# Optimization experiments

Measured on AMD Instinct MI355X. Metric: run time of the kernel, lower is better.

## Reference

```python
import jax, jax.numpy as jnp
import numpy as np

TEMP = 1.0  # composition softmax temperature

def _bank_topk(x, U, V, logits, top_k):
    # softmax over primitive logits, select top-k, renormalize, fused low-rank projection
    w = jax.nn.softmax(logits / TEMP)                     # [P]
    tw, ti = jax.lax.top_k(w, top_k)                      # [k], [k]
    tw = tw / tw.sum()
    Us = U[ti]                                            # [k, d_in, r]
    Vs = V[ti]                                            # [k, r, d_out]
    h = jnp.einsum('bsd,kdr->bksr', x, Us)                # low-rank bottleneck
    return jnp.einsum('bksr,kro,k->bso', h, Vs, tw)       # weighted fuse

def reference(x, q_U, q_V, k_U, k_V, v_U, v_V, q_logits, k_logits, v_logits, out_w, top_k):
    B, S, _ = x.shape
    H, D = 16, 64
    q = _bank_topk(x, q_U, q_V, q_logits, top_k)
    k = _bank_topk(x, k_U, k_V, k_logits, top_k)
    v = _bank_topk(x, v_U, v_V, v_logits, top_k)
    q = q.reshape(B, S, H, D).transpose(0, 2, 1, 3)       # [B,H,S,D]
    k = k.reshape(B, S, H, D).transpose(0, 2, 1, 3)
    v = v.reshape(B, S, H, D).transpose(0, 2, 1, 3)
    scale = 1.0 / jnp.sqrt(jnp.asarray(D, dtype=x.dtype))
    scores = jnp.einsum('bhqd,bhkd->bhqk', q, k) * scale  # [B,H,S,S]
    causal = jnp.triu(jnp.ones((S, S), dtype=bool), 1)
    scores = jnp.where(causal[None, None], jnp.finfo(x.dtype).min, scores)
    probs = jax.nn.softmax(scores, axis=-1)
    out = jnp.einsum('bhqk,bhkd->bhqd', probs, v)
    out = out.transpose(0, 2, 1, 3).reshape(B, S, H * D)
    return out @ out_w.T                                   # nn.Linear(H*D, d_model, bias=False)

def setup_inputs() -> dict:
    key = jax.random.key(0)
    ks = jax.random.split(key, 11)
    P, d, r = 16, 1024, 64
    B, S = 4, 1024
    f = jnp.float32
    inp = {
        'x': jax.random.normal(ks[0], (B, S, d), f),
        'q_U': jax.random.normal(ks[1], (P, d, r), f) * (1.0 / np.sqrt(d)),
        'q_V': jax.random.normal(ks[2], (P, r, d), f) * (1.0 / np.sqrt(r)),
        'k_U': jax.random.normal(ks[3], (P, d, r), f) * (1.0 / np.sqrt(d)),
        'k_V': jax.random.normal(ks[4], (P, r, d), f) * (1.0 / np.sqrt(r)),
        'v_U': jax.random.normal(ks[5], (P, d, r), f) * (1.0 / np.sqrt(d)),
        'v_V': jax.random.normal(ks[6], (P, r, d), f) * (1.0 / np.sqrt(r)),
        'q_logits': jax.random.normal(ks[7], (P,), f) * 0.01,
        'k_logits': jax.random.normal(ks[8], (P,), f) * 0.01,
        'v_logits': jax.random.normal(ks[9], (P,), f) * 0.01,
        'out_w': jax.random.normal(ks[10], (d, d), f) * (1.0 / np.sqrt(d)),
        'top_k': 4,
    }
    return inp
```

## Files before the change

kernel.cpp:

```cpp
#include <hip/hip_runtime.h>
#include <math.h>

#define D_MODEL 1024
#define RANK    64
#define PMAX    16
#define S_LEN   1024
#define HD      64
#define MROWS   4096
#define NHEAD   16
#define BATCH   4

typedef short short8v __attribute__((ext_vector_type(8)));
typedef float floatx4 __attribute__((ext_vector_type(4)));

typedef __attribute__((address_space(1))) const unsigned int* gptr_t;
typedef __attribute__((address_space(3))) unsigned int* lptr_t;

static __device__ __forceinline__ void async16(const void* g, void* l) {
    __builtin_amdgcn_global_load_lds((gptr_t)g, (lptr_t)l, 16, 0, 0);
}

static __device__ __forceinline__ short f2bf(float f) {
    unsigned int u = __float_as_uint(f);
    u = (u + 0x7fffu + ((u >> 16) & 1u)) >> 16;
    return (short)u;
}

__global__ void topk_weights_kernel(const float* __restrict__ ql,
                                    const float* __restrict__ kl,
                                    const float* __restrict__ vl,
                                    const int* __restrict__ topk,
                                    int* __restrict__ idx_out,
                                    float* __restrict__ w_out) {
    int bank = threadIdx.x;
    if (bank >= 3) return;
    const float* lg = (bank == 0) ? ql : (bank == 1) ? kl : vl;
    int K = *topk; if (K < 1) K = 1; if (K > PMAX) K = PMAX;
    float l[PMAX];
    for (int i = 0; i < PMAX; ++i) l[i] = lg[i];
    bool used[PMAX];
    for (int i = 0; i < PMAX; ++i) used[i] = false;
    int   sel_i[PMAX];
    float sel_l[PMAX];
    for (int j = 0; j < K; ++j) {
        int best = -1; float bv = -INFINITY;
        for (int i = 0; i < PMAX; ++i)
            if (!used[i] && l[i] > bv) { bv = l[i]; best = i; }
        used[best] = true; sel_i[j] = best; sel_l[j] = bv;
    }
    float mx = sel_l[0];
    float e[PMAX];
    float sum = 0.f;
    for (int j = 0; j < K; ++j) { e[j] = __expf(sel_l[j] - mx); sum += e[j]; }
    float inv = 1.f / sum;
    for (int j = 0; j < PMAX; ++j) {
        idx_out[bank * PMAX + j] = (j < K) ? sel_i[j] : 0;
        w_out[bank * PMAX + j]   = (j < K) ? e[j] * inv : 0.f;
    }
}

__global__ __launch_bounds__(256) void convert_bf16_kernel(
    const float* __restrict__ src, short* __restrict__ dst, int n4) {
    int i = blockIdx.x * 256 + threadIdx.x;
    if (i < n4) {
        float4 f = ((const float4*)src)[i];
        short4 o;
        o.x = f2bf(f.x); o.y = f2bf(f.y); o.z = f2bf(f.z); o.w = f2bf(f.w);
        ((short4*)dst)[i] = o;
    }
}

__global__ __launch_bounds__(256) void prep_uv_kernel(
    const float* __restrict__ qU, const float* __restrict__ kU,
    const float* __restrict__ vU,
    const float* __restrict__ qV, const float* __restrict__ kV,
    const float* __restrict__ vV,
    const int* __restrict__ idx, const float* __restrict__ wsel,
    short* __restrict__ Ut, short* __restrict__ Vt) {
    int z    = blockIdx.z;
    int j    = blockIdx.y;
    int tile = blockIdx.x;
    int t    = threadIdx.x;
    __shared__ float T[64][65];
    int bank = (z < 3) ? z : z - 3;
    int p = idx[bank * PMAX + j];

    if (z < 3) {
        const float* U = (bank == 0) ? qU : (bank == 1) ? kU : vU;
        const float* src = U + (size_t)p * D_MODEL * RANK;
        int d0 = tile * 64;
        int rl = t & 63, dq = t >> 6;
#pragma unroll
        for (int i = 0; i < 16; ++i) {
            int dl = i * 4 + dq;
            T[rl][dl] = src[(size_t)(d0 + dl) * RANK + rl];
        }
        __syncthreads();
        short* dst = Ut + (size_t)bank * D_MODEL * D_MODEL;
        int rr = t >> 2;
#pragma unroll
        for (int i = 0; i < 4; ++i) {
            int c = (t & 3) * 16 + i * 4;
            short4 o;
            o.x = f2bf(T[rr][c + 0]); o.y = f2bf(T[rr][c + 1]);
            o.z = f2bf(T[rr][c + 2]); o.w = f2bf(T[rr][c + 3]);
            *(short4*)&dst[(size_t)(j * 64 + rr) * D_MODEL + d0 + c] = o;
        }
    } else {
        const float* V = (bank == 0) ? qV : (bank == 1) ? kV : vV;
        float wj = wsel[bank * PMAX + j];
        const float* src = V + (size_t)p * RANK * D_MODEL;
        int n0 = tile * 64;
        int nl = t & 63, rq = t >> 6;
#pragma unroll
        for (int i = 0; i < 16; ++i) {
            int rl = i * 4 + rq;
            T[nl][rl] = src[(size_t)rl * D_MODEL + n0 + nl] * wj;
        }
        __syncthreads();
        short* dst = Vt + (size_t)bank * D_MODEL * D_MODEL;
        int rr = t >> 2;
#pragma unroll
        for (int i = 0; i < 4; ++i) {
            int c = (t & 3) * 16 + i * 4;
            short4 o;
            o.x = f2bf(T[rr][c + 0]); o.y = f2bf(T[rr][c + 1]);
            o.z = f2bf(T[rr][c + 2]); o.w = f2bf(T[rr][c + 3]);
            *(short4*)&dst[(size_t)(n0 + rr) * D_MODEL + j * 64 + c] = o;
        }
    }
}

static __device__ __forceinline__ void mfma_gemm_tile(
    const short* __restrict__ A, const short* __restrict__ B, int kl,
    int m0, int n0, short* As, short* Bs, floatx4 acc[4][4]) {
    const int t    = threadIdx.x;
    const int w    = t >> 6;
    const int lane = t & 63;
    const int wm   = w & 1, wn = w >> 1;
    const int colL = lane & 15, quad = lane >> 4;
    const int srow  = lane >> 2;
    const int skoff = (lane & 3) * 8;

#pragma unroll
    for (int i = 0; i < 4; ++i)
#pragma unroll
        for (int j = 0; j < 4; ++j) acc[i][j] = (floatx4){0.f, 0.f, 0.f, 0.f};

    for (int k0 = 0; k0 < kl; k0 += 32) {
        async16(A + (size_t)(m0 + w * 16 + srow) * D_MODEL + k0 + skoff,
                As + (w * 16 + srow) * 32 + skoff);
        async16(A + (size_t)(m0 + 64 + w * 16 + srow) * D_MODEL + k0 + skoff,
                As + (64 + w * 16 + srow) * 32 + skoff);
        async16(B + (size_t)(n0 + w * 16 + srow) * D_MODEL + k0 + skoff,
                Bs + (w * 16 + srow) * 32 + skoff);
        async16(B + (size_t)(n0 + 64 + w * 16 + srow) * D_MODEL + k0 + skoff,
                Bs + (64 + w * 16 + srow) * 32 + skoff);
        __syncthreads();
        short8v af[4], bf[4];
#pragma unroll
        for (int i = 0; i < 4; ++i)
            af[i] = *(const short8v*)&As[(wm * 64 + i * 16 + colL) * 32 + quad * 8];
#pragma unroll
        for (int j = 0; j < 4; ++j)
            bf[j] = *(const short8v*)&Bs[(wn * 64 + j * 16 + colL) * 32 + quad * 8];
#pragma unroll
        for (int i = 0; i < 4; ++i)
#pragma unroll
            for (int j = 0; j < 4; ++j)
                acc[i][j] = __builtin_amdgcn_mfma_f32_16x16x32_bf16(af[i], bf[j], acc[i][j], 0, 0, 0);
        __syncthreads();
    }
}

__global__ __launch_bounds__(256) void gemm_h_kernel(
    const short* __restrict__ xb, const short* __restrict__ Ut,
    const int* __restrict__ topk, short* __restrict__ h) {
    int K = *topk; if (K < 1) K = 1; if (K > PMAX) K = PMAX;
    int n0 = blockIdx.y * 128;
    if (n0 >= K * 64) return;
    int m0 = blockIdx.x * 128;
    int bank = blockIdx.z;
    __shared__ short As[128 * 32];
    __shared__ short Bs[128 * 32];
    floatx4 acc[4][4];
    mfma_gemm_tile(xb, Ut + (size_t)bank * D_MODEL * D_MODEL, D_MODEL, m0, n0, As, Bs, acc);

    const int t = threadIdx.x, w = t >> 6, lane = t & 63;
    const int wm = w & 1, wn = w >> 1, colL = lane & 15, quad = lane >> 4;
    short* H = h + (size_t)bank * MROWS * D_MODEL;
#pragma unroll
    for (int i = 0; i < 4; ++i)
#pragma unroll
        for (int j = 0; j < 4; ++j)
#pragma unroll
            for (int r = 0; r < 4; ++r)
                H[(size_t)(m0 + wm * 64 + i * 16 + quad * 4 + r) * D_MODEL +
                  (n0 + wn * 64 + j * 16 + colL)] = f2bf(acc[i][j][r]);
}

__global__ __launch_bounds__(256) void gemm_qkv_kernel(
    const short* __restrict__ h, const short* __restrict__ Vt,
    const int* __restrict__ topk, short* __restrict__ qkv) {
    int K = *topk; if (K < 1) K = 1; if (K > PMAX) K = PMAX;
    int m0 = blockIdx.x * 128;
    int n0 = blockIdx.y * 128;
    int bank = blockIdx.z;
    __shared__ short As[128 * 32];
    __shared__ short Bs[128 * 32];
    floatx4 acc[4][4];
    mfma_gemm_tile(h + (size_t)bank * MROWS * D_MODEL,
                   Vt + (size_t)bank * D_MODEL * D_MODEL, K * 64, m0, n0, As, Bs, acc);

    const int t = threadIdx.x, w = t >> 6, lane = t & 63;
    const int wm = w & 1, wn = w >> 1, colL = lane & 15, quad = lane >> 4;
    short* outp = qkv + (size_t)bank * MROWS * D_MODEL;
    const float scl = (bank == 0) ? 0.18033688f : 1.0f;
#pragma unroll
    for (int i = 0; i < 4; ++i)
#pragma unroll
        for (int j = 0; j < 4; ++j)
#pragma unroll
            for (int r = 0; r < 4; ++r) {
                int m = m0 + wm * 64 + i * 16 + quad * 4 + r;
                int n = n0 + wn * 64 + j * 16 + colL;
                int b = m >> 10, s = m & 1023;
                int head = n >> 6, d = n & 63;
                outp[(((size_t)(b * NHEAD + head) << 10) + s) * HD + d] = f2bf(acc[i][j][r] * scl);
            }
}

__global__ __launch_bounds__(256) void transpose_v_kernel(
    const short* __restrict__ src, short* __restrict__ dst) {
    int st = blockIdx.x, bh = blockIdx.y;
    __shared__ short T[64][72];
    const short* S = src + (size_t)bh * (S_LEN * HD) + (size_t)st * 64 * HD;
    int r = threadIdx.x >> 2, i = threadIdx.x & 3;
    *(short8v*)&T[r][i * 16]     = *(const short8v*)&S[r * HD + i * 16];
    *(short8v*)&T[r][i * 16 + 8] = *(const short8v*)&S[r * HD + i * 16 + 8];
    __syncthreads();
    short* Drow = dst + (size_t)bh * (S_LEN * HD) + (size_t)r * S_LEN + st * 64 + i * 16;
    short8v o0, o1;
#pragma unroll
    for (int k = 0; k < 8; ++k) o0[k] = T[i * 16 + k][r];
#pragma unroll
    for (int k = 0; k < 8; ++k) o1[k] = T[i * 16 + 8 + k][r];
    *(short8v*)&Drow[0] = o0;
    *(short8v*)&Drow[8] = o1;
}

static __device__ __forceinline__ void stage_tiles(
    const short* __restrict__ Kg, const short* __restrict__ Vg, int jt,
    short* KsB, short* VsB, int w, int lane) {
#pragma unroll
    for (int q = 0; q < 2; ++q) {
        int c   = q * 64 + lane;
        int r16 = c >> 3;
        int i   = c & 7;
        int r   = w * 16 + r16;
        int g   = i ^ (r16 & 7);
        async16(Kg + (size_t)(jt * 64 + r) * HD + g * 8, KsB + r * 64 + i * 8);
        async16(Vg + (size_t)r * S_LEN + jt * 64 + g * 8, VsB + r * 64 + i * 8);
    }
}

template<bool DIAG>
static __device__ __forceinline__ void attn_step(
    const short* KsB, const short* VsB, short* Pw,
    short8v aq0, short8v aq1, int w, int col, int quad,
    floatx4& O0, floatx4& O1, floatx4& O2, floatx4& O3,
    float mrow[4], float lrow[4]) {
    const int colLow = col & 7;
    floatx4 c4[4];
#pragma unroll
    for (int n = 0; n < 4; ++n) {
        if (!DIAG || n <= w) {
            floatx4 z = {0.f, 0.f, 0.f, 0.f};
            short8v b0 = *(const short8v*)&KsB[(n * 16 + col) * 64 + ((quad ^ colLow) << 3)];
            short8v b1 = *(const short8v*)&KsB[(n * 16 + col) * 64 + (((quad + 4) ^ colLow) << 3)];
            z = __builtin_amdgcn_mfma_f32_16x16x32_bf16(aq0, b0, z, 0, 0, 0);
            z = __builtin_amdgcn_mfma_f32_16x16x32_bf16(aq1, b1, z, 0, 0, 0);
            if (DIAG) {
#pragma unroll
                for (int r = 0; r < 4; ++r)
                    if (n == w && col > quad * 4 + r) z[r] = -INFINITY;
            }
            c4[n] = z;
        } else {
            c4[n] = (floatx4){-INFINITY, -INFINITY, -INFINITY, -INFINITY};
        }
    }
#pragma unroll
    for (int r = 0; r < 4; ++r) {
        float tm = fmaxf(fmaxf(c4[0][r], c4[1][r]), fmaxf(c4[2][r], c4[3][r]));
        tm = fmaxf(tm, __shfl_xor(tm, 1));
        tm = fmaxf(tm, __shfl_xor(tm, 2));
        tm = fmaxf(tm, __shfl_xor(tm, 4));
        tm = fmaxf(tm, __shfl_xor(tm, 8));
        float mnew  = fmaxf(mrow[r], tm);
        float alpha = exp2f(mrow[r] - mnew);
        float p0 = exp2f(c4[0][r] - mnew), p1 = exp2f(c4[1][r] - mnew);
        float p2 = exp2f(c4[2][r] - mnew), p3 = exp2f(c4[3][r] - mnew);
        lrow[r] = lrow[r] * alpha + (p0 + p1 + p2 + p3);
        mrow[r] = mnew;
        O0[r] *= alpha; O1[r] *= alpha; O2[r] *= alpha; O3[r] *= alpha;
        short* pr = Pw + (quad * 4 + r) * 72 + col;
        pr[0]  = f2bf(p0); pr[16] = f2bf(p1);
        pr[32] = f2bf(p2); pr[48] = f2bf(p3);
    }
    const int ksmax = DIAG ? (w >> 1) : 1;
#pragma unroll
    for (int ks = 0; ks < 2; ++ks) {
        if (ks > ksmax) break;
        short8v ap = *(const short8v*)&Pw[col * 72 + ks * 32 + quad * 8];
        int pc = ((ks * 4 + quad) ^ colLow) << 3;
        short8v v0 = *(const short8v*)&VsB[(0  + col) * 64 + pc];
        short8v v1 = *(const short8v*)&VsB[(16 + col) * 64 + pc];
        short8v v2 = *(const short8v*)&VsB[(32 + col) * 64 + pc];
        short8v v3 = *(const short8v*)&VsB[(48 + col) * 64 + pc];
        O0 = __builtin_amdgcn_mfma_f32_16x16x32_bf16(ap, v0, O0, 0, 0, 0);
        O1 = __builtin_amdgcn_mfma_f32_16x16x32_bf16(ap, v1, O1, 0, 0, 0);
        O2 = __builtin_amdgcn_mfma_f32_16x16x32_bf16(ap, v2, O2, 0, 0, 0);
        O3 = __builtin_amdgcn_mfma_f32_16x16x32_bf16(ap, v3, O3, 0, 0, 0);
    }
}

__global__ __launch_bounds__(256) void attn_mfma_kernel(
    const short* __restrict__ qkv,
    const short* __restrict__ vtb,
    short* __restrict__ attn_out) {
    const int t    = threadIdx.x;
    const int w    = t >> 6;
    const int lane = t & 63;
    const int col  = lane & 15;
    const int quad = lane >> 4;
    const int pr   = blockIdx.x;
    const int bh   = blockIdx.y;
    const size_t HS   = (size_t)S_LEN * HD;
    const size_t BSTR = (size_t)MROWS * D_MODEL;
    const short* Qg = qkv + (size_t)bh * HS;
    const short* Kg = qkv + BSTR + (size_t)bh * HS;
    const short* Vg = vtb + (size_t)bh * HS;

    __shared__ short Ks[2][4096];
    __shared__ short Vs[2][4096];
    __shared__ short Ps[4][16 * 72];
    short* Pw = &Ps[w][0];

    for (int ph = 0; ph < 2; ++ph) {
        const int qt = ph ? (15 - pr) : pr;
        const int qrow = qt * 64 + w * 16 + col;
        short8v aq0 = *(const short8v*)(Qg + (size_t)qrow * HD + quad * 8);
        short8v aq1 = *(const short8v*)(Qg + (size_t)qrow * HD + 32 + quad * 8);
        floatx4 O0 = {0.f, 0.f, 0.f, 0.f}, O1 = O0, O2 = O0, O3 = O0;
        float mrow[4] = {-INFINITY, -INFINITY, -INFINITY, -INFINITY};
        float lrow[4] = {0.f, 0.f, 0.f, 0.f};

        __syncthreads();
        stage_tiles(Kg, Vg, 0, Ks[0], Vs[0], w, lane);
        __syncthreads();
        int cur = 0;
        for (int jt = 0; jt < qt; ++jt) {
            stage_tiles(Kg, Vg, jt + 1, Ks[cur ^ 1], Vs[cur ^ 1], w, lane);
            attn_step<false>(Ks[cur], Vs[cur], Pw, aq0, aq1, w, col, quad,
                             O0, O1, O2, O3, mrow, lrow);
            __syncthreads();
            cur ^= 1;
        }
        attn_step<true>(Ks[cur], Vs[cur], Pw, aq0, aq1, w, col, quad,
                        O0, O1, O2, O3, mrow, lrow);

        const int b  = bh >> 4;
        const int hh = bh & 15;
        short* orow = attn_out +
            ((size_t)(b * S_LEN) + qt * 64 + w * 16) * D_MODEL + hh * 64;
#pragma unroll
        for (int r = 0; r < 4; ++r) {
            float l = lrow[r];
            l += __shfl_xor(l, 1); l += __shfl_xor(l, 2);
            l += __shfl_xor(l, 4); l += __shfl_xor(l, 8);
            float inv = 1.f / l;
            short* prw = orow + (size_t)(quad * 4 + r) * D_MODEL;
            prw[0  + col] = f2bf(O0[r] * inv);
            prw[16 + col] = f2bf(O1[r] * inv);
            prw[32 + col] = f2bf(O2[r] * inv);
            prw[48 + col] = f2bf(O3[r] * inv);
        }
    }
}

__global__ __launch_bounds__(256) void gemm_proj_kernel(
    const short* __restrict__ attnb, const short* __restrict__ wb,
    float* __restrict__ outp) {
    int m0 = blockIdx.x * 128;
    int n0 = blockIdx.y * 128;
    __shared__ short As[128 * 32];
    __shared__ short Bs[128 * 32];
    floatx4 acc[4][4];
    mfma_gemm_tile(attnb, wb, D_MODEL, m0, n0, As, Bs, acc);

    const int t = threadIdx.x, w = t >> 6, lane = t & 63;
    const int wm = w & 1, wn = w >> 1, colL = lane & 15, quad = lane >> 4;
#pragma unroll
    for (int i = 0; i < 4; ++i)
#pragma unroll
        for (int j = 0; j < 4; ++j)
#pragma unroll
            for (int r = 0; r < 4; ++r)
                outp[(size_t)(m0 + wm * 64 + i * 16 + quad * 4 + r) * D_MODEL +
                     (n0 + wn * 64 + j * 16 + colL)] = acc[i][j][r];
}

extern "C" void kernel_launch(void* const* d_in, const int* in_sizes, int n_in,
                              void* d_out, int out_size, void* d_ws, size_t ws_size,
                              hipStream_t stream) {
    const float* x    = (const float*)d_in[0];
    const float* qU   = (const float*)d_in[1];
    const float* qV   = (const float*)d_in[2];
    const float* kU   = (const float*)d_in[3];
    const float* kV   = (const float*)d_in[4];
    const float* vU   = (const float*)d_in[5];
    const float* vV   = (const float*)d_in[6];
    const float* qlg  = (const float*)d_in[7];
    const float* klg  = (const float*)d_in[8];
    const float* vlg  = (const float*)d_in[9];
    const float* outw = (const float*)d_in[10];
    const int*   topk = (const int*)d_in[11];
    float* outp = (float*)d_out;

    char* ws = (char*)d_ws;
    int*   idxp = (int*)ws;
    float* wp   = (float*)(ws + 256);
    short* xb   = (short*)(ws + 512);
    short* Ut   = xb + (size_t)MROWS * D_MODEL;
    short* Vt   = Ut + (size_t)3 * D_MODEL * D_MODEL;
    short* wb   = Vt + (size_t)3 * D_MODEL * D_MODEL;
    short* hbuf = wb + (size_t)D_MODEL * D_MODEL;
    short* qkvb = hbuf + (size_t)3 * MROWS * D_MODEL;
    short* attnb = qkvb + (size_t)3 * MROWS * D_MODEL;
    short* vtb  = attnb + (size_t)MROWS * D_MODEL;

    topk_weights_kernel<<<1, 64, 0, stream>>>(qlg, klg, vlg, topk, idxp, wp);
    convert_bf16_kernel<<<(MROWS * D_MODEL / 4 + 255) / 256, 256, 0, stream>>>(
        x, xb, MROWS * D_MODEL / 4);
    convert_bf16_kernel<<<(D_MODEL * D_MODEL / 4 + 255) / 256, 256, 0, stream>>>(
        outw, wb, D_MODEL * D_MODEL / 4);
    prep_uv_kernel<<<dim3(16, 16, 6), 256, 0, stream>>>(
        qU, kU, vU, qV, kV, vV, idxp, wp, Ut, Vt);
    gemm_h_kernel<<<dim3(32, 8, 3), 256, 0, stream>>>(xb, Ut, topk, hbuf);
    gemm_qkv_kernel<<<dim3(32, 8, 3), 256, 0, stream>>>(hbuf, Vt, topk, qkvb);
    transpose_v_kernel<<<dim3(16, 64), 256, 0, stream>>>(
        qkvb + (size_t)2 * MROWS * D_MODEL, vtb);
    attn_mfma_kernel<<<dim3(8, 64), 256, 0, stream>>>(qkvb, vtb, attnb);
    gemm_proj_kernel<<<dim3(32, 8), 256, 0, stream>>>(attnb, wb, outp);
}
```

Baseline: 231.3 us.

## Fuse prep kernels, double-buffer GEMM tiles, and widen attention key chunks

Merges the top-k selection, both bf16 conversions and the U/V preparation into one launch, with each prep block recomputing its own top-k choice so the separate topk kernel goes away. The GEMM main loop is double-buffered, prefetching the next K slice into a second LDS buffer while MFMAs run on the current one. The attention kernel now processes 128-key chunks per stage instead of 64, with a new V layout and swizzle. Together these cut launch count and per-step barriers, at the cost of twice the LDS per block, which may lower occupancy.

New measurement: 252.6 us. 9.2% more time.

```diff
diff --git a/kernel.cpp b/kernel.cpp
--- a/kernel.cpp
+++ b/kernel.cpp
@@ -26,65 +26,70 @@
     return (short)u;
 }
 
-__global__ void topk_weights_kernel(const float* __restrict__ ql,
-                                    const float* __restrict__ kl,
-                                    const float* __restrict__ vl,
-                                    const int* __restrict__ topk,
-                                    int* __restrict__ idx_out,
-                                    float* __restrict__ w_out) {
-    int bank = threadIdx.x;
-    if (bank >= 3) return;
-    const float* lg = (bank == 0) ? ql : (bank == 1) ? kl : vl;
-    int K = *topk; if (K < 1) K = 1; if (K > PMAX) K = PMAX;
+static __device__ __forceinline__ void topk_select(
+    const float* __restrict__ lg, int K, int j, int* p_out, float* w_out) {
     float l[PMAX];
+#pragma unroll
     for (int i = 0; i < PMAX; ++i) l[i] = lg[i];
     bool used[PMAX];
+#pragma unroll
     for (int i = 0; i < PMAX; ++i) used[i] = false;
-    int   sel_i[PMAX];
-    float sel_l[PMAX];
-    for (int j = 0; j < K; ++j) {
+    float first = 0.f, sum = 0.f, sl = 0.f;
+    int sel = 0;
+    for (int jj = 0; jj < K; ++jj) {
         int best = -1; float bv = -INFINITY;
         for (int i = 0; i < PMAX; ++i)
             if (!used[i] && l[i] > bv) { bv = l[i]; best = i; }
-        used[best] = true; sel_i[j] = best; sel_l[j] = bv;
-    }
-    float mx = sel_l[0];
-    float e[PMAX];
-    float sum = 0.f;
-    for (int j = 0; j < K; ++j) { e[j] = __expf(sel_l[j] - mx); sum += e[j]; }
-    float inv = 1.f / sum;
-    for (int j = 0; j < PMAX; ++j) {
-        idx_out[bank * PMAX + j] = (j < K) ? sel_i[j] : 0;
-        w_out[bank * PMAX + j]   = (j < K) ? e[j] * inv : 0.f;
-    }
-}
-
-__global__ __launch_bounds__(256) void convert_bf16_kernel(
-    const float* __restrict__ src, short* __restrict__ dst, int n4) {
-    int i = blockIdx.x * 256 + threadIdx.x;
-    if (i < n4) {
-        float4 f = ((const float4*)src)[i];
-        short4 o;
-        o.x = f2bf(f.x); o.y = f2bf(f.y); o.z = f2bf(f.z); o.w = f2bf(f.w);
-        ((short4*)dst)[i] = o;
-    }
-}
-
-__global__ __launch_bounds__(256) void prep_uv_kernel(
+        used[best] = true;
+        if (jj == 0) first = bv;
+        float e = __expf(bv - first);
+        sum += e;
+        if (jj == j) { sel = best; sl = e; }
+    }
+    if (j < K) { *p_out = sel; *w_out = sl / sum; }
+    else       { *p_out = 0;   *w_out = 0.f; }
+}
+
+__global__ __launch_bounds__(256) void prep_all_kernel(
+    const float* __restrict__ x,
     const float* __restrict__ qU, const float* __restrict__ kU,
     const float* __restrict__ vU,
     const float* __restrict__ qV, const float* __restrict__ kV,
     const float* __restrict__ vV,
-    const int* __restrict__ idx, const float* __restrict__ wsel,
+    const float* __restrict__ qlg, const float* __restrict__ klg,
+    const float* __restrict__ vlg,
+    const int* __restrict__ topk, const float* __restrict__ outw,
+    short* __restrict__ xb, short* __restrict__ wb,
     short* __restrict__ Ut, short* __restrict__ Vt) {
-    int z    = blockIdx.z;
-    int j    = blockIdx.y;
-    int tile = blockIdx.x;
-    int t    = threadIdx.x;
+    int b = blockIdx.x;
+    int t = threadIdx.x;
+    if (b < 4096) {
+        int i = b * 256 + t;
+        float4 f = ((const float4*)x)[i];
+        short4 o;
+        o.x = f2bf(f.x); o.y = f2bf(f.y); o.z = f2bf(f.z); o.w = f2bf(f.w);
+        ((short4*)xb)[i] = o;
+        return;
+    }
+    if (b < 5120) {
+        int i = (b - 4096) * 256 + t;
+        float4 f = ((const float4*)outw)[i];
+        short4 o;
+        o.x = f2bf(f.x); o.y = f2bf(f.y); o.z = f2bf(f.z); o.w = f2bf(f.w);
+        ((short4*)wb)[i] = o;
+        return;
+    }
+    int rem  = b - 5120;
+    int z    = rem >> 8;
+    int j    = (rem >> 4) & 15;
+    int tile = rem & 15;
+    int bank = (z < 3) ? z : z - 3;
+    int K = *topk; if (K < 1) K = 1; if (K > PMAX) K = PMAX;
+    const float* lg = (bank == 0) ? qlg : (bank == 1) ? klg : vlg;
+    int p; float wj;
+    topk_select(lg, K, j, &p, &wj);
+
     __shared__ float T[64][65];
-    int bank = (z < 3) ? z : z - 3;
-    int p = idx[bank * PMAX + j];
-
     if (z < 3) {
         const float* U = (bank == 0) ? qU : (bank == 1) ? kU : vU;
         const float* src = U + (size_t)p * D_MODEL * RANK;
@@ -108,7 +113,6 @@
         }
     } else {
         const float* V = (bank == 0) ? qV : (bank == 1) ? kV : vV;
-        float wj = wsel[bank * PMAX + j];
         const float* src = V + (size_t)p * RANK * D_MODEL;
         int n0 = tile * 64;
         int nl = t & 63, rq = t >> 6;
@@ -129,6 +133,20 @@
             *(short4*)&dst[(size_t)(n0 + rr) * D_MODEL + j * 64 + c] = o;
         }
     }
+}
+
+static __device__ __forceinline__ void gemm_stage(
+    const short* __restrict__ A, const short* __restrict__ B,
+    int m0, int n0, int k0, short* Ab, short* Bb,
+    int w, int srow, int skoff) {
+    async16(A + (size_t)(m0 + w * 16 + srow) * D_MODEL + k0 + skoff,
+            Ab + (w * 16 + srow) * 32 + skoff);
+    async16(A + (size_t)(m0 + 64 + w * 16 + srow) * D_MODEL + k0 + skoff,
+            Ab + (64 + w * 16 + srow) * 32 + skoff);
+    async16(B + (size_t)(n0 + w * 16 + srow) * D_MODEL + k0 + skoff,
+            Bb + (w * 16 + srow) * 32 + skoff);
+    async16(B + (size_t)(n0 + 64 + w * 16 + srow) * D_MODEL + k0 + skoff,
+            Bb + (64 + w * 16 + srow) * 32 + skoff);
 }
 
 static __device__ __forceinline__ void mfma_gemm_tile(
@@ -147,29 +165,31 @@
 #pragma unroll
         for (int j = 0; j < 4; ++j) acc[i][j] = (floatx4){0.f, 0.f, 0.f, 0.f};
 
-    for (int k0 = 0; k0 < kl; k0 += 32) {
-        async16(A + (size_t)(m0 + w * 16 + srow) * D_MODEL + k0 + skoff,
-                As + (w * 16 + srow) * 32 + skoff);
-        async16(A + (size_t)(m0 + 64 + w * 16 + srow) * D_MODEL + k0 + skoff,
-                As + (64 + w * 16 + srow) * 32 + skoff);
-        async16(B + (size_t)(n0 + w * 16 + srow) * D_MODEL + k0 + skoff,
-                Bs + (w * 16 + srow) * 32 + skoff);
-        async16(B + (size_t)(n0 + 64 + w * 16 + srow) * D_MODEL + k0 + skoff,
-                Bs + (64 + w * 16 + srow) * 32 + skoff);
-        __syncthreads();
+    gemm_stage(A, B, m0, n0, 0, As, Bs, w, srow, skoff);
+    __syncthreads();
+    const int nk = kl >> 5;
+    int cur = 0;
+    for (int kt = 0; kt < nk; ++kt) {
+        if (kt + 1 < nk)
+            gemm_stage(A, B, m0, n0, (kt + 1) * 32,
+                       As + ((cur ^ 1) << 12), Bs + ((cur ^ 1) << 12),
+                       w, srow, skoff);
+        const short* Ab = As + (cur << 12);
+        const short* Bb = Bs + (cur << 12);
         short8v af[4], bf[4];
 #pragma unroll
         for (int i = 0; i < 4; ++i)
-            af[i] = *(const short8v*)&As[(wm * 64 + i * 16 + colL) * 32 + quad * 8];
+            af[i] = *(const short8v*)&Ab[(wm * 64 + i * 16 + colL) * 32 + quad * 8];
 #pragma unroll
         for (int j = 0; j < 4; ++j)
-            bf[j] = *(const short8v*)&Bs[(wn * 64 + j * 16 + colL) * 32 + quad * 8];
+            bf[j] = *(const short8v*)&Bb[(wn * 64 + j * 16 + colL) * 32 + quad * 8];
 #pragma unroll
         for (int i = 0; i < 4; ++i)
 #pragma unroll
             for (int j = 0; j < 4; ++j)
                 acc[i][j] = __builtin_amdgcn_mfma_f32_16x16x32_bf16(af[i], bf[j], acc[i][j], 0, 0, 0);
         __syncthreads();
+        cur ^= 1;
     }
 }
 
@@ -181,8 +201,8 @@
     if (n0 >= K * 64) return;
     int m0 = blockIdx.x * 128;
     int bank = blockIdx.z;
-    __shared__ short As[128 * 32];
-    __shared__ short Bs[128 * 32];
+    __shared__ short As[8192];
+    __shared__ short Bs[8192];
     floatx4 acc[4][4];
     mfma_gemm_tile(xb, Ut + (size_t)bank * D_MODEL * D_MODEL, D_MODEL, m0, n0, As, Bs, acc);
 
@@ -206,8 +226,8 @@
     int m0 = blockIdx.x * 128;
     int n0 = blockIdx.y * 128;
     int bank = blockIdx.z;
-    __shared__ short As[128 * 32];
-    __shared__ short Bs[128 * 32];
+    __shared__ short As[8192];
+    __shared__ short Bs[8192];
     floatx4 acc[4][4];
     mfma_gemm_tile(h + (size_t)bank * MROWS * D_MODEL,
                    Vt + (size_t)bank * D_MODEL * D_MODEL, K * 64, m0, n0, As, Bs, acc);
@@ -249,79 +269,105 @@
     *(short8v*)&Drow[8] = o1;
 }
 
-static __device__ __forceinline__ void stage_tiles(
-    const short* __restrict__ Kg, const short* __restrict__ Vg, int jt,
+static __device__ __forceinline__ void attn_stage(
+    const short* __restrict__ Kg, const short* __restrict__ Vg, int base,
     short* KsB, short* VsB, int w, int lane) {
 #pragma unroll
-    for (int q = 0; q < 2; ++q) {
-        int c   = q * 64 + lane;
-        int r16 = c >> 3;
-        int i   = c & 7;
-        int r   = w * 16 + r16;
-        int g   = i ^ (r16 & 7);
-        async16(Kg + (size_t)(jt * 64 + r) * HD + g * 8, KsB + r * 64 + i * 8);
-        async16(Vg + (size_t)r * S_LEN + jt * 64 + g * 8, VsB + r * 64 + i * 8);
-    }
-}
-
-template<bool DIAG>
+    for (int q2 = 0; q2 < 4; ++q2) {
+        int row = w * 32 + q2 * 8 + (lane >> 3);
+        int i   = lane & 7;
+        int g   = i ^ (row & 7);
+        async16(Kg + (size_t)(base + row) * HD + g * 8, KsB + row * 64 + i * 8);
+    }
+#pragma unroll
+    for (int q2 = 0; q2 < 4; ++q2) {
+        int d    = w * 16 + q2 * 4 + (lane >> 4);
+        int i    = lane & 15;
+        int half = i >> 3, i3 = i & 7;
+        int g3   = i3 ^ (d & 7);
+        async16(Vg + (size_t)d * S_LEN + base + half * 64 + g3 * 8,
+                VsB + d * 128 + i * 8);
+    }
+}
+
+template<int NN, bool DIAG>
 static __device__ __forceinline__ void attn_step(
     const short* KsB, const short* VsB, short* Pw,
     short8v aq0, short8v aq1, int w, int col, int quad,
     floatx4& O0, floatx4& O1, floatx4& O2, floatx4& O3,
     float mrow[4], float lrow[4]) {
-    const int colLow = col & 7;
-    floatx4 c4[4];
-#pragma unroll
-    for (int n = 0; n < 4; ++n) {
-        if (!DIAG || n <= w) {
+    const int cl7 = col & 7;
+    float sc[NN][4];
+#pragma unroll
+    for (int n = 0; n < NN; ++n) {
+        const int dn = n - (NN - 4);
+        if (DIAG && dn > w) {
+#pragma unroll
+            for (int r = 0; r < 4; ++r) sc[n][r] = -INFINITY;
+        } else {
             floatx4 z = {0.f, 0.f, 0.f, 0.f};
-            short8v b0 = *(const short8v*)&KsB[(n * 16 + col) * 64 + ((quad ^ colLow) << 3)];
-            short8v b1 = *(const short8v*)&KsB[(n * 16 + col) * 64 + (((quad + 4) ^ colLow) << 3)];
+            const short* kb = KsB + (n * 16 + col) * 64;
+            short8v b0 = *(const short8v*)(kb + ((quad ^ cl7) << 3));
+            short8v b1 = *(const short8v*)(kb + (((quad + 4) ^ cl7) << 3));
             z = __builtin_amdgcn_mfma_f32_16x16x32_bf16(aq0, b0, z, 0, 0, 0);
             z = __builtin_amdgcn_mfma_f32_16x16x32_bf16(aq1, b1, z, 0, 0, 0);
-            if (DIAG) {
+            if (DIAG && dn == w) {
 #pragma unroll
                 for (int r = 0; r < 4; ++r)
-                    if (n == w && col > quad * 4 + r) z[r] = -INFINITY;
+                    if (col > quad * 4 + r) z[r] = -INFINITY;
             }
-            c4[n] = z;
-        } else {
-            c4[n] = (floatx4){-INFINITY, -INFINITY, -INFINITY, -INFINITY};
-        }
-    }
+#pragma unroll
+            for (int r = 0; r < 4; ++r) sc[n][r] = z[r];
+        }
+    }
+    float pv[NN][4];
 #pragma unroll
     for (int r = 0; r < 4; ++r) {
-        float tm = fmaxf(fmaxf(c4[0][r], c4[1][r]), fmaxf(c4[2][r], c4[3][r]));
+        float tm = sc[0][r];
+#pragma unroll
+        for (int n = 1; n < NN; ++n) tm = fmaxf(tm, sc[n][r]);
         tm = fmaxf(tm, __shfl_xor(tm, 1));
         tm = fmaxf(tm, __shfl_xor(tm, 2));
         tm = fmaxf(tm, __shfl_xor(tm, 4));
         tm = fmaxf(tm, __shfl_xor(tm, 8));
         float mnew  = fmaxf(mrow[r], tm);
         float alpha = exp2f(mrow[r] - mnew);
-        float p0 = exp2f(c4[0][r] - mnew), p1 = exp2f(c4[1][r] - mnew);
-        float p2 = exp2f(c4[2][r] - mnew), p3 = exp2f(c4[3][r] - mnew);
-        lrow[r] = lrow[r] * alpha + (p0 + p1 + p2 + p3);
+        float ps = 0.f;
+#pragma unroll
+        for (int n = 0; n < NN; ++n) {
+            float p = exp2f(sc[n][r] - mnew);
+            pv[n][r] = p;
+            ps += p;
+        }
+        lrow[r] = lrow[r] * alpha + ps;
         mrow[r] = mnew;
         O0[r] *= alpha; O1[r] *= alpha; O2[r] *= alpha; O3[r] *= alpha;
-        short* pr = Pw + (quad * 4 + r) * 72 + col;
-        pr[0]  = f2bf(p0); pr[16] = f2bf(p1);
-        pr[32] = f2bf(p2); pr[48] = f2bf(p3);
-    }
-    const int ksmax = DIAG ? (w >> 1) : 1;
-#pragma unroll
-    for (int ks = 0; ks < 2; ++ks) {
-        if (ks > ksmax) break;
-        short8v ap = *(const short8v*)&Pw[col * 72 + ks * 32 + quad * 8];
-        int pc = ((ks * 4 + quad) ^ colLow) << 3;
-        short8v v0 = *(const short8v*)&VsB[(0  + col) * 64 + pc];
-        short8v v1 = *(const short8v*)&VsB[(16 + col) * 64 + pc];
-        short8v v2 = *(const short8v*)&VsB[(32 + col) * 64 + pc];
-        short8v v3 = *(const short8v*)&VsB[(48 + col) * 64 + pc];
-        O0 = __builtin_amdgcn_mfma_f32_16x16x32_bf16(ap, v0, O0, 0, 0, 0);
-        O1 = __builtin_amdgcn_mfma_f32_16x16x32_bf16(ap, v1, O1, 0, 0, 0);
-        O2 = __builtin_amdgcn_mfma_f32_16x16x32_bf16(ap, v2, O2, 0, 0, 0);
-        O3 = __builtin_amdgcn_mfma_f32_16x16x32_bf16(ap, v3, O3, 0, 0, 0);
+    }
+#pragma unroll
+    for (int h = 0; h < NN / 4; ++h) {
+#pragma unroll
+        for (int n2 = 0; n2 < 4; ++n2)
+#pragma unroll
+            for (int r = 0; r < 4; ++r)
+                Pw[(quad * 4 + r) * 72 + n2 * 16 + col] = f2bf(pv[h * 4 + n2][r]);
+        const int kslim = DIAG ? ((NN - 4 + w) >> 1) : 3;
+#pragma unroll
+        for (int ks2 = 2 * h; ks2 < 2 * h + 2; ++ks2) {
+            if (DIAG && ks2 > kslim) break;
+            short8v ap = *(const short8v*)(Pw + col * 72 + (ks2 & 1) * 32 + quad * 8);
+            const int half = ks2 >> 1;
+            const int i3   = (ks2 & 1) * 4 + quad;
+            const int swz  = ((i3 ^ cl7) << 3);
+            const short* vb = VsB + half * 64 + swz;
+            short8v v0 = *(const short8v*)(vb + (0  + col) * 128);
+            short8v v1 = *(const short8v*)(vb + (16 + col) * 128);
+            short8v v2 = *(const short8v*)(vb + (32 + col) * 128);
+            short8v v3 = *(const short8v*)(vb + (48 + col) * 128);
+            O0 = __builtin_amdgcn_mfma_f32_16x16x32_bf16(ap, v0, O0, 0, 0, 0);
+            O1 = __builtin_amdgcn_mfma_f32_16x16x32_bf16(ap, v1, O1, 0, 0, 0);
+            O2 = __builtin_amdgcn_mfma_f32_16x16x32_bf16(ap, v2, O2, 0, 0, 0);
+            O3 = __builtin_amdgcn_mfma_f32_16x16x32_bf16(ap, v3, O3, 0, 0, 0);
+        }
     }
 }
 
@@ -342,10 +388,10 @@
     const short* Kg = qkv + BSTR + (size_t)bh * HS;
     const short* Vg = vtb + (size_t)bh * HS;
 
-    __shared__ short Ks[2][4096];
-    __shared__ short Vs[2][4096];
-    __shared__ short Ps[4][16 * 72];
-    short* Pw = &Ps[w][0];
+    __shared__ short Ks[2][8192];
+    __shared__ short Vs[2][8192];
+    __shared__ short Ps[4][1152];
+    short* Pw = Ps[w];
 
     for (int ph = 0; ph < 2; ++ph) {
         const int qt = ph ? (15 - pr) : pr;
@@ -356,19 +402,24 @@
         float mrow[4] = {-INFINITY, -INFINITY, -INFINITY, -INFINITY};
         float lrow[4] = {0.f, 0.f, 0.f, 0.f};
 
+        const int nC = (qt + 2) >> 1;
         __syncthreads();
-        stage_tiles(Kg, Vg, 0, Ks[0], Vs[0], w, lane);
+        attn_stage(Kg, Vg, 0, Ks[0], Vs[0], w, lane);
         __syncthreads();
         int cur = 0;
-        for (int jt = 0; jt < qt; ++jt) {
-            stage_tiles(Kg, Vg, jt + 1, Ks[cur ^ 1], Vs[cur ^ 1], w, lane);
-            attn_step<false>(Ks[cur], Vs[cur], Pw, aq0, aq1, w, col, quad,
-                             O0, O1, O2, O3, mrow, lrow);
+        for (int c = 0; c + 1 < nC; ++c) {
+            attn_stage(Kg, Vg, (c + 1) * 128, Ks[cur ^ 1], Vs[cur ^ 1], w, lane);
+            attn_step<8, false>(Ks[cur], Vs[cur], Pw, aq0, aq1, w, col, quad,
+                                O0, O1, O2, O3, mrow, lrow);
             __syncthreads();
             cur ^= 1;
         }
-        attn_step<true>(Ks[cur], Vs[cur], Pw, aq0, aq1, w, col, quad,
-                        O0, O1, O2, O3, mrow, lrow);
+        if (qt & 1)
+            attn_step<8, true>(Ks[cur], Vs[cur], Pw, aq0, aq1, w, col, quad,
+                               O0, O1, O2, O3, mrow, lrow);
+        else
+            attn_step<4, true>(Ks[cur], Vs[cur], Pw, aq0, aq1, w, col, quad,
+                               O0, O1, O2, O3, mrow, lrow);
 
         const int b  = bh >> 4;
         const int hh = bh & 15;
@@ -394,8 +445,8 @@
     float* __restrict__ outp) {
     int m0 = blockIdx.x * 128;
     int n0 = blockIdx.y * 128;
-    __shared__ short As[128 * 32];
-    __shared__ short Bs[128 * 32];
+    __shared__ short As[8192];
+    __shared__ short Bs[8192];
     floatx4 acc[4][4];
     mfma_gemm_tile(attnb, wb, D_MODEL, m0, n0, As, Bs, acc);
 
@@ -429,9 +480,7 @@
     float* outp = (float*)d_out;
 
     char* ws = (char*)d_ws;
-    int*   idxp = (int*)ws;
-    float* wp   = (float*)(ws + 256);
-    short* xb   = (short*)(ws + 512);
+    short* xb   = (short*)ws;
     short* Ut   = xb + (size_t)MROWS * D_MODEL;
     short* Vt   = Ut + (size_t)3 * D_MODEL * D_MODEL;
     short* wb   = Vt + (size_t)3 * D_MODEL * D_MODEL;
@@ -440,13 +489,8 @@
     short* attnb = qkvb + (size_t)3 * MROWS * D_MODEL;
     short* vtb  = attnb + (size_t)MROWS * D_MODEL;
 
-    topk_weights_kernel<<<1, 64, 0, stream>>>(qlg, klg, vlg, topk, idxp, wp);
-    convert_bf16_kernel<<<(MROWS * D_MODEL / 4 + 255) / 256, 256, 0, stream>>>(
-        x, xb, MROWS * D_MODEL / 4);
-    convert_bf16_kernel<<<(D_MODEL * D_MODEL / 4 + 255) / 256, 256, 0, stream>>>(
-        outw, wb, D_MODEL * D_MODEL / 4);
-    prep_uv_kernel<<<dim3(16, 16, 6), 256, 0, stream>>>(
-        qU, kU, vU, qV, kV, vV, idxp, wp, Ut, Vt);
+    prep_all_kernel<<<6656, 256, 0, stream>>>(
+        x, qU, kU, vU, qV, kV, vV, qlg, klg, vlg, topk, outw, xb, wb, Ut, Vt);
     gemm_h_kernel<<<dim3(32, 8, 3), 256, 0, stream>>>(xb, Ut, topk, hbuf);
     gemm_qkv_kernel<<<dim3(32, 8, 3), 256, 0, stream>>>(hbuf, Vt, topk, qkvb);
     transpose_v_kernel<<<dim3(16, 64), 256, 0, stream>>>(
```
